# Kernel optimization log

Hardware: AMD Instinct MI355X
Metric: run time of the kernel (lower is better)

## Reference

```python
import jax, jax.numpy as jnp
import numpy as np

N_SUPPORT = 32768
N_QUERY = 16384
D = 512
K = 32
U = 128
NEG_BIG = -1e30  # masked-out attention logit; all-masked class -> uniform weights == mean fallback


def setup_inputs() -> dict:
    key = jax.random.key(0)
    k1, k2, k3, k4, k5 = jax.random.split(key, 5)
    query = jax.random.normal(k1, (N_QUERY, D), dtype=jnp.float32)
    support = jax.random.normal(k2, (N_SUPPORT, D), dtype=jnp.float32)
    labels = jax.random.randint(k3, (N_SUPPORT,), 0, K, dtype=jnp.int32)
    # Xavier-normal-ish init for per-class projection V (U,D) and attention vector w (U,1)
    V = jax.random.normal(k4, (K, U, D), dtype=jnp.float32) * np.float32(np.sqrt(2.0 / (U + D)))
    w = jax.random.normal(k5, (K, U), dtype=jnp.float32) * np.float32(np.sqrt(2.0 / (U + 1)))
    return {"query_embeddings": query, "support_embeddings": support,
            "support_labels": labels, "V": V, "w": w}


def reference(query_embeddings, support_embeddings, support_labels, V, w):
    # --- attention-weighted prototypes (vectorized over classes via masked softmax) ---
    # projected[k,n,u] = tanh(V[k] @ x_n)
    projected = jnp.tanh(jnp.einsum('nd,kud->knu', support_embeddings, V))
    attn_logits = jnp.einsum('knu,ku->kn', projected, w)              # (K, N)
    mask = support_labels[None, :] == jnp.arange(K, dtype=support_labels.dtype)[:, None]
    attn_logits = jnp.where(mask, attn_logits, NEG_BIG)
    # per-class softmax over support samples; an empty class yields uniform weights,
    # i.e. prototype = mean(embeddings) -- exactly the torch fallback branch.
    attn = jax.nn.softmax(attn_logits, axis=1)                        # (K, N)
    prototypes = jnp.einsum('kn,nd->kd', attn, support_embeddings)    # (K, D)

    # --- squared-euclidean distance classification ---
    q2 = jnp.sum(query_embeddings * query_embeddings, axis=1, keepdims=True)   # (B, 1)
    p2 = jnp.sum(prototypes * prototypes, axis=1)[None, :]                     # (1, K)
    dists = q2 + p2 - 2.0 * (query_embeddings @ prototypes.T)                  # (B, K)
    return jax.nn.log_softmax(-dists, axis=1)
```

## Files before the change

kernel.cpp:

```cpp
#include <hip/hip_runtime.h>
#include <hip/hip_bf16.h>

#define N_SUPPORT 32768
#define N_QUERY   16384
#define DIM       512
#define NCLS      32
#define NU        128
#define NBLK      (N_SUPPORT / 256)

#define OFF_IDX      0
#define OFF_COUNT    131072
#define OFF_START    131200
#define OFF_M        131456
#define OFF_Z        131584
#define OFF_P2       131712
#define OFF_LOGIT    132096
#define OFF_PRAW     263168
#define OFF_PROTO    328704
#define OFF_BHIST    394240
#define OFF_BOFFS    410624
#define OFF_VBF      458752
#define OFF_PBF      4653056

typedef __attribute__((ext_vector_type(8))) short short8;
typedef __attribute__((ext_vector_type(4))) short short4v;
typedef __attribute__((ext_vector_type(4))) float f32x4;

__device__ inline unsigned short f2bf(float f) {
    unsigned int x = __builtin_bit_cast(unsigned int, f);
    unsigned int r = x + 0x7fffu + ((x >> 16) & 1u);
    return (unsigned short)(r >> 16);
}
__device__ inline float bf2f(unsigned short h) {
    unsigned int u = ((unsigned int)h) << 16;
    return __builtin_bit_cast(float, u);
}

__device__ inline short8 pack_bf8(float4 f0, float4 f1) {
    short8 pk;
    pk[0] = f2bf(f0.x); pk[1] = f2bf(f0.y); pk[2] = f2bf(f0.z); pk[3] = f2bf(f0.w);
    pk[4] = f2bf(f1.x); pk[5] = f2bf(f1.y); pk[6] = f2bf(f1.z); pk[7] = f2bf(f1.w);
    return pk;
}

__device__ inline void pack_hilo(float4 f0, float4 f1, short8& hi, short8& lo) {
    float v[8] = {f0.x, f0.y, f0.z, f0.w, f1.x, f1.y, f1.z, f1.w};
    #pragma unroll
    for (int i = 0; i < 8; i++) {
        unsigned short h = f2bf(v[i]);
        hi[i] = (short)h;
        lo[i] = (short)f2bf(v[i] - bf2f(h));
    }
}

__global__ void k_vcast(const float* __restrict__ V, short* __restrict__ Vbf,
                        float* __restrict__ praw, const int* __restrict__ labels,
                        int* __restrict__ bhist) {
    __shared__ int h[NCLS];
    int tid = threadIdx.x;
    bool dohist = (blockIdx.x < NBLK);
    if (dohist) {
        if (tid < NCLS) h[tid] = 0;
        __syncthreads();
        atomicAdd(&h[labels[blockIdx.x * 256 + tid]], 1);
    }
    int i = blockIdx.x * 256 + tid;
    int ob = i * 4;
    int j0  = ob & 7;
    int s   = (ob >> 3) & 7;
    int u   = (ob >> 6) & 127;
    int c   = (ob >> 13) & 7;
    int k   = ob >> 16;
    int d   = c * 64 + ((s ^ (u & 7)) * 8) + j0;
    float4 f = *(const float4*)(V + ((size_t)(k * 128 + u) * DIM + d));
    short4v o;
    o[0] = f2bf(f.x); o[1] = f2bf(f.y); o[2] = f2bf(f.z); o[3] = f2bf(f.w);
    *(short4v*)(Vbf + (size_t)ob) = o;
    if (i < (NCLS * DIM) / 4) *(float4*)(praw + i * 4) = make_float4(0.f, 0.f, 0.f, 0.f);
    if (dohist) {
        __syncthreads();
        if (tid < NCLS) bhist[blockIdx.x * NCLS + tid] = h[tid];
    }
}

__global__ void k_scan2(const int* __restrict__ bhist, int* __restrict__ boffs,
                        int* __restrict__ start, int* __restrict__ count) {
    __shared__ int tot[NCLS];
    int tid = threadIdx.x;
    if (tid < NCLS) {
        int s = 0;
        for (int b = 0; b < NBLK; b++) {
            boffs[b * NCLS + tid] = s;
            s += bhist[b * NCLS + tid];
        }
        tot[tid] = s;
    }
    __syncthreads();
    if (tid == 0) {
        int run = 0;
        for (int k = 0; k < NCLS; k++) {
            start[k] = run;
            count[k] = tot[k];
            run += tot[k];
        }
        start[NCLS] = run;
    }
}

__global__ void k_scatter(const int* __restrict__ labels, const int* __restrict__ boffs,
                          const int* __restrict__ start, int* __restrict__ idx_c) {
    __shared__ int whist[4][NCLS];
    int tid = threadIdx.x;
    int n = blockIdx.x * 256 + tid;
    int l = labels[n];
    int lane = tid & 63, wid = tid >> 6;
    unsigned long long mymask = 0ull;
    #pragma unroll
    for (int k = 0; k < NCLS; k++) {
        unsigned long long mk = __ballot(l == k);
        if (k == l) mymask = mk;
        if (lane == k) whist[wid][k] = __popcll(mk);
    }
    int rank = __popcll(mymask & ((1ull << lane) - 1ull));
    __syncthreads();
    int wbase = 0;
    for (int w = 0; w < wid; w++) wbase += whist[w][l];
    idx_c[start[l] + boffs[blockIdx.x * NCLS + l] + wbase + rank] = n;
}

__launch_bounds__(256, 1)
__global__ void k_logits(const float* __restrict__ support, const short* __restrict__ Vbf,
                         const float* __restrict__ w, const int* __restrict__ idx_c,
                         const int* __restrict__ start, const int* __restrict__ count,
                         float* __restrict__ logit_c) {
    int k = blockIdx.y;
    int cnt = count[k];
    int base = blockIdx.x * 32;
    if (base >= cnt) return;
    int M = min(32, cnt - base);
    int s0 = start[k] + base;
    int t = threadIdx.x;

    __shared__ __align__(16) short Xs[32 * 512];
    __shared__ float part[4][32];

    int l = t & 63, wv = t >> 6;
    int lo16 = l & 15, hi4 = l >> 4;

    float4 xf[8][2];
    #pragma unroll
    for (int rep = 0; rep < 8; rep++) {
        int row = wv + 4 * rep;
        int r = (row < M) ? row : 0;
        int nidx = idx_c[s0 + r];
        const float* src = support + (size_t)nidx * DIM + l * 8;
        xf[rep][0] = *(const float4*)src;
        xf[rep][1] = *(const float4*)(src + 4);
    }

    const short* Vk = Vbf + (size_t)k * (8 * 128 * 64);
    short8 vreg[4][2][2];
    #pragma unroll
    for (int c = 0; c < 4; c++)
        #pragma unroll
        for (int ks = 0; ks < 2; ks++)
            #pragma unroll
            for (int nt = 0; nt < 2; nt++) {
                int u = wv * 32 + nt * 16 + lo16;
                int q = ks * 4 + hi4;
                vreg[c][ks][nt] = *(const short8*)(Vk + (size_t)c * 8192 + (size_t)u * 64 + ((q ^ (u & 7)) * 8));
            }

    #pragma unroll
    for (int rep = 0; rep < 8; rep++) {
        int row = wv + 4 * rep;
        *(short8*)&Xs[row * 512 + ((l ^ (row & 7)) * 8)] = pack_bf8(xf[rep][0], xf[rep][1]);
    }

    f32x4 acc[2][2];
    #pragma unroll
    for (int mt = 0; mt < 2; mt++)
        #pragma unroll
        for (int nt = 0; nt < 2; nt++) acc[mt][nt] = (f32x4){0.f, 0.f, 0.f, 0.f};

    __syncthreads();

#define COMPUTE(c, vb) { _Pragma("unroll")                                        \
    for (int ks = 0; ks < 2; ks++) {                                              \
        short8 a[2];                                                              \
        _Pragma("unroll")                                                         \
        for (int mt = 0; mt < 2; mt++) {                                          \
            int ar = mt * 16 + lo16;                                              \
            int cu = (c) * 8 + ks * 4 + hi4;                                      \
            a[mt] = *(short8*)&Xs[ar * 512 + ((cu ^ (ar & 7)) * 8)];              \
        }                                                                         \
        _Pragma("unroll")                                                         \
        for (int mt = 0; mt < 2; mt++)                                            \
            _Pragma("unroll")                                                     \
            for (int nt = 0; nt < 2; nt++)                                        \
                acc[mt][nt] = __builtin_amdgcn_mfma_f32_16x16x32_bf16(a[mt], vb[ks][nt], acc[mt][nt], 0, 0, 0); \
    } }

    #pragma unroll
    for (int c = 0; c < 4; c++) COMPUTE(c, vreg[c]);

    #pragma unroll
    for (int c = 0; c < 4; c++)
        #pragma unroll
        for (int ks = 0; ks < 2; ks++)
            #pragma unroll
            for (int nt = 0; nt < 2; nt++) {
                int u = wv * 32 + nt * 16 + lo16;
                int q = ks * 4 + hi4;
                vreg[c][ks][nt] = *(const short8*)(Vk + (size_t)(c + 4) * 8192 + (size_t)u * 64 + ((q ^ (u & 7)) * 8));
            }
    #pragma unroll
    for (int c = 0; c < 4; c++) COMPUTE(c + 4, vreg[c]);
#undef COMPUTE

    float w0 = w[k * NU + wv * 32 + lo16];
    float w1 = w[k * NU + wv * 32 + 16 + lo16];
    #pragma unroll
    for (int mt = 0; mt < 2; mt++) {
        #pragma unroll
        for (int r = 0; r < 4; r++) {
            float val = tanhf(acc[mt][0][r]) * w0 + tanhf(acc[mt][1][r]) * w1;
            val += __shfl_xor(val, 1);
            val += __shfl_xor(val, 2);
            val += __shfl_xor(val, 4);
            val += __shfl_xor(val, 8);
            if (lo16 == 0) part[wv][mt * 16 + hi4 * 4 + r] = val;
        }
    }
    __syncthreads();
    if (t < M) {
        logit_c[s0 + t] = part[0][t] + part[1][t] + part[2][t] + part[3][t];
    }
}

__global__ void k_mz(const float* __restrict__ logit_c, const int* __restrict__ start,
                     const int* __restrict__ count, float* __restrict__ m, float* __restrict__ Z) {
    int k = blockIdx.x;
    int cnt = count[k], s0 = start[k];
    int tid = threadIdx.x;
    __shared__ float red[256];
    float mx = -1e30f;
    for (int i = tid; i < cnt; i += 256) mx = fmaxf(mx, logit_c[s0 + i]);
    red[tid] = mx; __syncthreads();
    for (int off = 128; off > 0; off >>= 1) {
        if (tid < off) red[tid] = fmaxf(red[tid], red[tid + off]);
        __syncthreads();
    }
    float mk = red[0];
    __syncthreads();
    float s = 0.f;
    for (int i = tid; i < cnt; i += 256) s += expf(logit_c[s0 + i] - mk);
    red[tid] = s; __syncthreads();
    for (int off = 128; off > 0; off >>= 1) {
        if (tid < off) red[tid] += red[tid + off];
        __syncthreads();
    }
    if (tid == 0) { m[k] = mk; Z[k] = red[0]; }
}

__launch_bounds__(512, 1)
__global__ void k_proto(const float* __restrict__ support, const int* __restrict__ idx_c,
                        const float* __restrict__ logit_c, const int* __restrict__ start,
                        const int* __restrict__ count, const float* __restrict__ m,
                        float* __restrict__ praw) {
    int k = blockIdx.y;
    int cnt = count[k];
    int base = blockIdx.x * 64;
    if (base >= cnt) return;
    int M = min(64, cnt - base);
    int s0 = start[k] + base;
    __shared__ float wts[64];
    __shared__ int sid[64];
    int t = threadIdx.x;
    if (t < 64) {
        sid[t] = idx_c[s0 + ((t < M) ? t : 0)];
        wts[t] = (t < M) ? expf(logit_c[s0 + t] - m[k]) : 0.f;
    }
    __syncthreads();
    int d = t;
    float a = 0.f;
    for (int s = 0; s < 64; s += 4) {
        float r0 = support[(size_t)sid[s + 0] * DIM + d];
        float r1 = support[(size_t)sid[s + 1] * DIM + d];
        float r2 = support[(size_t)sid[s + 2] * DIM + d];
        float r3 = support[(size_t)sid[s + 3] * DIM + d];
        a += wts[s] * r0 + wts[s + 1] * r1 + wts[s + 2] * r2 + wts[s + 3] * r3;
    }
    atomicAdd(&praw[k * DIM + d], a);
}

__global__ void k_protonorm(const float* __restrict__ support, const float* __restrict__ praw,
                            const float* __restrict__ Z, const int* __restrict__ count,
                            float* __restrict__ proto, float* __restrict__ p2,
                            short* __restrict__ Pbf) {
    int k = blockIdx.x;
    int tid = threadIdx.x;
    int cnt = count[k];
    __shared__ float red[256];
    float pv[2];
    if (cnt > 0) {
        float inv = 1.f / Z[k];
        #pragma unroll
        for (int i = 0; i < 2; i++) pv[i] = praw[k * DIM + tid + i * 256] * inv;
    } else {
        #pragma unroll
        for (int i = 0; i < 2; i++) {
            int d = tid + i * 256;
            float s = 0.f;
            for (int n = 0; n < N_SUPPORT; n++) s += support[(size_t)n * DIM + d];
            pv[i] = s * (1.f / N_SUPPORT);
        }
    }
    float acc = 0.f;
    #pragma unroll
    for (int i = 0; i < 2; i++) {
        int d = tid + i * 256;
        proto[k * DIM + d] = pv[i];
        acc += pv[i] * pv[i];
        int c = d >> 6, off = d & 63, o = off >> 3, j = off & 7;
        int s = o ^ (k & 7);
        int pos = (c * 32 + k) * 64 + s * 8 + j;
        unsigned short hi = f2bf(pv[i]);
        Pbf[pos] = (short)hi;
        Pbf[NCLS * DIM + pos] = (short)f2bf(pv[i] - bf2f(hi));
    }
    red[tid] = acc; __syncthreads();
    for (int off = 128; off > 0; off >>= 1) {
        if (tid < off) red[tid] += red[tid + off];
        __syncthreads();
    }
    if (tid == 0) p2[k] = red[0];
}

__launch_bounds__(256, 1)
__global__ void k_dist(const float* __restrict__ query, const short* __restrict__ Pbf,
                       const float* __restrict__ p2, float* __restrict__ out) {
    __shared__ __align__(16) short Ph[NCLS * DIM];
    __shared__ __align__(16) short Pl[NCLS * DIM];
    __shared__ __align__(16) short Qh[2][64 * 64];
    __shared__ __align__(16) short Ql[2][64 * 64];
    int t = threadIdx.x;
    int qbase = blockIdx.x * 64;
    int l = t & 63, wv = t >> 6;
    int lo16 = l & 15, hi4 = l >> 4;

    #pragma unroll
    for (int rep = 0; rep < 8; rep++) {
        int u = t + 256 * rep;
        ((short8*)Ph)[u] = ((const short8*)Pbf)[u];
        ((short8*)Pl)[u] = ((const short8*)(Pbf + NCLS * DIM))[u];
    }

    int qrow[2], qslot[2], qdst[2];
    const float* qsrc[2];
    #pragma unroll
    for (int rep = 0; rep < 2; rep++) {
        int u = t + 256 * rep;
        qrow[rep] = u >> 3; qslot[rep] = u & 7;
        qdst[rep] = qrow[rep] * 64 + ((qslot[rep] ^ (qrow[rep] & 7)) * 8);
        qsrc[rep] = query + (size_t)(qbase + qrow[rep]) * DIM + qslot[rep] * 8;
    }

    f32x4 acc[2];
    acc[0] = (f32x4){0.f, 0.f, 0.f, 0.f};
    acc[1] = (f32x4){0.f, 0.f, 0.f, 0.f};

    float4 qa[2][2], qb[2][2];
#define LOADQ(d, c) { _Pragma("unroll") for (int rep = 0; rep < 2; rep++) { \
        d[rep][0] = *(const float4*)(qsrc[rep] + (c) * 64);                 \
        d[rep][1] = *(const float4*)(qsrc[rep] + (c) * 64 + 4); } }
#define WRITEQ(buf, d) { _Pragma("unroll") for (int rep = 0; rep < 2; rep++) { \
        short8 hi8, lo8;                                                        \
        pack_hilo(d[rep][0], d[rep][1], hi8, lo8);                              \
        *(short8*)&Qh[buf][qdst[rep]] = hi8;                                    \
        *(short8*)&Ql[buf][qdst[rep]] = lo8; } }

    LOADQ(qa, 0);
    LOADQ(qb, 1);
    WRITEQ(0, qa);

    for (int c = 0; c < 8; ++c) {
        int cur = c & 1;
        __syncthreads();
        if (c + 2 < 8) {
            if (cur == 0) { LOADQ(qa, c + 2); }
            else          { LOADQ(qb, c + 2); }
        }
        #pragma unroll
        for (int ks = 0; ks < 2; ks++) {
            int arow = wv * 16 + lo16;
            int asw = ((ks * 4 + hi4) ^ (arow & 7)) * 8;
            short8 ah = *(short8*)&Qh[cur][arow * 64 + asw];
            short8 al = *(short8*)&Ql[cur][arow * 64 + asw];
            #pragma unroll
            for (int nt = 0; nt < 2; nt++) {
                int brow = nt * 16 + lo16;
                int pos = (c * 32 + brow) * 64 + (((ks * 4 + hi4) ^ (brow & 7)) * 8);
                short8 bh = *(short8*)&Ph[pos];
                short8 bl = *(short8*)&Pl[pos];
                acc[nt] = __builtin_amdgcn_mfma_f32_16x16x32_bf16(ah, bh, acc[nt], 0, 0, 0);
                acc[nt] = __builtin_amdgcn_mfma_f32_16x16x32_bf16(ah, bl, acc[nt], 0, 0, 0);
                acc[nt] = __builtin_amdgcn_mfma_f32_16x16x32_bf16(al, bh, acc[nt], 0, 0, 0);
            }
        }
        if (c < 7) {
            if (cur == 0) { WRITEQ(1, qb); }
            else          { WRITEQ(0, qa); }
        }
    }
#undef LOADQ
#undef WRITEQ

    float p2v0 = p2[lo16];
    float p2v1 = p2[16 + lo16];
    #pragma unroll
    for (int r = 0; r < 4; r++) {
        float l0 = 2.f * acc[0][r] - p2v0;
        float l1 = 2.f * acc[1][r] - p2v1;
        float mx = fmaxf(l0, l1);
        mx = fmaxf(mx, __shfl_xor(mx, 1));
        mx = fmaxf(mx, __shfl_xor(mx, 2));
        mx = fmaxf(mx, __shfl_xor(mx, 4));
        mx = fmaxf(mx, __shfl_xor(mx, 8));
        float s = expf(l0 - mx) + expf(l1 - mx);
        s += __shfl_xor(s, 1);
        s += __shfl_xor(s, 2);
        s += __shfl_xor(s, 4);
        s += __shfl_xor(s, 8);
        float lse = mx + logf(s);
        int q = qbase + wv * 16 + hi4 * 4 + r;
        out[(size_t)q * NCLS + lo16] = l0 - lse;
        out[(size_t)q * NCLS + 16 + lo16] = l1 - lse;
    }
}

extern "C" void kernel_launch(void* const* d_in, const int* in_sizes, int n_in,
                              void* d_out, int out_size, void* d_ws, size_t ws_size,
                              hipStream_t stream) {
    const float* query   = (const float*)d_in[0];
    const float* support = (const float*)d_in[1];
    const int*   labels  = (const int*)d_in[2];
    const float* V       = (const float*)d_in[3];
    const float* w       = (const float*)d_in[4];
    float* out = (float*)d_out;
    char* ws = (char*)d_ws;

    int*   idx_c   = (int*)(ws + OFF_IDX);
    int*   count   = (int*)(ws + OFF_COUNT);
    int*   start   = (int*)(ws + OFF_START);
    float* m       = (float*)(ws + OFF_M);
    float* Z       = (float*)(ws + OFF_Z);
    float* p2      = (float*)(ws + OFF_P2);
    float* logit_c = (float*)(ws + OFF_LOGIT);
    float* praw    = (float*)(ws + OFF_PRAW);
    float* proto   = (float*)(ws + OFF_PROTO);
    int*   bhist   = (int*)(ws + OFF_BHIST);
    int*   boffs   = (int*)(ws + OFF_BOFFS);
    short* vbf     = (short*)(ws + OFF_VBF);
    short* pbf     = (short*)(ws + OFF_PBF);

    hipLaunchKernelGGL(k_vcast, dim3((NCLS * NU * DIM) / 1024), dim3(256), 0, stream,
                       V, vbf, praw, labels, bhist);
    hipLaunchKernelGGL(k_scan2, dim3(1), dim3(64), 0, stream, bhist, boffs, start, count);
    hipLaunchKernelGGL(k_scatter, dim3(NBLK), dim3(256), 0, stream, labels, boffs, start, idx_c);
    hipLaunchKernelGGL(k_logits, dim3(64, NCLS), dim3(256), 0, stream,
                       support, vbf, w, idx_c, start, count, logit_c);
    hipLaunchKernelGGL(k_mz, dim3(NCLS), dim3(256), 0, stream, logit_c, start, count, m, Z);
    hipLaunchKernelGGL(k_proto, dim3(32, NCLS), dim3(512), 0, stream,
                       support, idx_c, logit_c, start, count, m, praw);
    hipLaunchKernelGGL(k_protonorm, dim3(NCLS), dim3(256), 0, stream,
                       support, praw, Z, count, proto, p2, pbf);
    hipLaunchKernelGGL(k_dist, dim3(N_QUERY / 64), dim3(256), 0, stream, query, pbf, p2, out);
}
```

Baseline: 72.08 us.

## Pre-gather support rows into class-sorted bf16 buffer and load via LDS DMA

Adds a k_gather kernel that converts support rows to bf16 once and writes them, already swizzled, in class-sorted order using an inverse index computed in k_scatter. k_logits then streams a contiguous slab of pre-converted rows straight into shared memory with global_load_lds, replacing its scattered fp32 gathers and per-block conversion. The aim is to cut the gather latency and register pressure in the logits GEMM. The cost is an extra kernel launch and an extra write and read of a 32 MB bf16 copy. The last tile of each class may now read rows that belong to the next class, which should be harmless only if those rows are masked later.

```diff
diff --git a/kernel.cpp b/kernel.cpp
--- a/kernel.cpp
+++ b/kernel.cpp
@@ -21,10 +21,15 @@
 #define OFF_BOFFS    410624
 #define OFF_VBF      458752
 #define OFF_PBF      4653056
+#define OFF_INV      4718592
+#define OFF_XS       4849664
 
 typedef __attribute__((ext_vector_type(8))) short short8;
 typedef __attribute__((ext_vector_type(4))) short short4v;
 typedef __attribute__((ext_vector_type(4))) float f32x4;
+
+typedef __attribute__((address_space(3))) unsigned int lds_u32;
+typedef const __attribute__((address_space(1))) unsigned int glb_u32;
 
 __device__ inline unsigned short f2bf(float f) {
     unsigned int x = __builtin_bit_cast(unsigned int, f);
@@ -108,7 +113,8 @@
 }
 
 __global__ void k_scatter(const int* __restrict__ labels, const int* __restrict__ boffs,
-                          const int* __restrict__ start, int* __restrict__ idx_c) {
+                          const int* __restrict__ start, int* __restrict__ idx_c,
+                          int* __restrict__ inv) {
     __shared__ int whist[4][NCLS];
     int tid = threadIdx.x;
     int n = blockIdx.x * 256 + tid;
@@ -125,12 +131,32 @@
     __syncthreads();
     int wbase = 0;
     for (int w = 0; w < wid; w++) wbase += whist[w][l];
-    idx_c[start[l] + boffs[blockIdx.x * NCLS + l] + wbase + rank] = n;
+    int pos = start[l] + boffs[blockIdx.x * NCLS + l] + wbase + rank;
+    idx_c[pos] = n;
+    inv[n] = (pos << 3) | ((pos - start[l]) & 7);
 }
 
 __launch_bounds__(256, 1)
-__global__ void k_logits(const float* __restrict__ support, const short* __restrict__ Vbf,
-                         const float* __restrict__ w, const int* __restrict__ idx_c,
+__global__ void k_gather(const float* __restrict__ support, const int* __restrict__ inv,
+                         short* __restrict__ xs) {
+    int t = threadIdx.x;
+    int l = t & 63, wv = t >> 6;
+    int rowbase = blockIdx.x * 64;
+    #pragma unroll 4
+    for (int i = 0; i < 16; i++) {
+        int n = rowbase + wv + 4 * i;
+        const float* src = support + (size_t)n * DIM + l * 8;
+        float4 f0 = *(const float4*)src;
+        float4 f1 = *(const float4*)(src + 4);
+        int iv = inv[n];
+        int pos = iv >> 3, swz = iv & 7;
+        *(short8*)&xs[(size_t)pos * 512 + ((l ^ swz) * 8)] = pack_bf8(f0, f1);
+    }
+}
+
+__launch_bounds__(256, 1)
+__global__ void k_logits(const short* __restrict__ xs, const short* __restrict__ Vbf,
+                         const float* __restrict__ w,
                          const int* __restrict__ start, const int* __restrict__ count,
                          float* __restrict__ logit_c) {
     int k = blockIdx.y;
@@ -147,15 +173,12 @@
     int l = t & 63, wv = t >> 6;
     int lo16 = l & 15, hi4 = l >> 4;
 
-    float4 xf[8][2];
+    const short* xsrc = xs + (size_t)s0 * 512;
     #pragma unroll
     for (int rep = 0; rep < 8; rep++) {
-        int row = wv + 4 * rep;
-        int r = (row < M) ? row : 0;
-        int nidx = idx_c[s0 + r];
-        const float* src = support + (size_t)nidx * DIM + l * 8;
-        xf[rep][0] = *(const float4*)src;
-        xf[rep][1] = *(const float4*)(src + 4);
+        int u = t + 256 * rep;
+        __builtin_amdgcn_global_load_lds((glb_u32*)(xsrc + (size_t)u * 8),
+                                         (lds_u32*)&Xs[u * 8], 16, 0, 0);
     }
 
     const short* Vk = Vbf + (size_t)k * (8 * 128 * 64);
@@ -170,12 +193,6 @@
                 int q = ks * 4 + hi4;
                 vreg[c][ks][nt] = *(const short8*)(Vk + (size_t)c * 8192 + (size_t)u * 64 + ((q ^ (u & 7)) * 8));
             }
-
-    #pragma unroll
-    for (int rep = 0; rep < 8; rep++) {
-        int row = wv + 4 * rep;
-        *(short8*)&Xs[row * 512 + ((l ^ (row & 7)) * 8)] = pack_bf8(xf[rep][0], xf[rep][1]);
-    }
 
     f32x4 acc[2][2];
     #pragma unroll
@@ -463,13 +480,16 @@
     int*   boffs   = (int*)(ws + OFF_BOFFS);
     short* vbf     = (short*)(ws + OFF_VBF);
     short* pbf     = (short*)(ws + OFF_PBF);
+    int*   inv     = (int*)(ws + OFF_INV);
+    short* xsorted = (short*)(ws + OFF_XS);
 
     hipLaunchKernelGGL(k_vcast, dim3((NCLS * NU * DIM) / 1024), dim3(256), 0, stream,
                        V, vbf, praw, labels, bhist);
     hipLaunchKernelGGL(k_scan2, dim3(1), dim3(64), 0, stream, bhist, boffs, start, count);
-    hipLaunchKernelGGL(k_scatter, dim3(NBLK), dim3(256), 0, stream, labels, boffs, start, idx_c);
+    hipLaunchKernelGGL(k_scatter, dim3(NBLK), dim3(256), 0, stream, labels, boffs, start, idx_c, inv);
+    hipLaunchKernelGGL(k_gather, dim3(N_SUPPORT / 64), dim3(256), 0, stream, support, inv, xsorted);
     hipLaunchKernelGGL(k_logits, dim3(64, NCLS), dim3(256), 0, stream,
-                       support, vbf, w, idx_c, start, count, logit_c);
+                       xsorted, vbf, w, start, count, logit_c);
     hipLaunchKernelGGL(k_mz, dim3(NCLS), dim3(256), 0, stream, logit_c, start, count, m, Z);
     hipLaunchKernelGGL(k_proto, dim3(32, NCLS), dim3(512), 0, stream,
                        support, idx_c, logit_c, start, count, m, praw);
```

Measured after the change: 83.58 us. 1.16x slower.
